# Performance work log

Measured on AMD Instinct MI355X. Metric: run time of the kernel, lower is better.

The kernel has to match this reference:

```python
import jax, jax.numpy as jnp
import numpy as np

GFD = 4096   # global feature dim (VGG fc7)
DH = 1024    # 2 * hidden_dim


def setup_inputs() -> dict:
    key = jax.random.key(0)
    ks = jax.random.split(key, 10)
    b, t_k = 32, 196
    s = lambda fan_in: 1.0 / np.sqrt(fan_in)
    return {
        "global_features": jax.random.normal(ks[0], (b, t_k, GFD), jnp.float32),
        "s_t_hat": jax.random.normal(ks[1], (b, DH), jnp.float32),
        "coverage_img": jnp.zeros((b, t_k, 1), jnp.float32),
        # params
        "Wg": jax.random.normal(ks[2], (GFD, GFD), jnp.float32) * s(GFD),
        "bg": jnp.zeros((GFD,), jnp.float32),
        "Gs": jax.random.normal(ks[3], (GFD, DH), jnp.float32) * s(GFD),
        "bgs": jnp.zeros((DH,), jnp.float32),
        "Wgs": jax.random.normal(ks[4], (DH, DH), jnp.float32) * s(DH),  # w_g_star, no bias
        "Wdec": jax.random.normal(ks[5], (DH, DH), jnp.float32) * s(DH),  # decode_proj
        "bdec": jnp.zeros((DH,), jnp.float32),
        "v": jax.random.normal(ks[6], (DH, 1), jnp.float32) * s(DH),  # score vector, no bias
    }


def reference(global_features, s_t_hat, coverage_img, Wg, bg, Gs, bgs, Wgs, Wdec, bdec, v):
    # g_star: project 4096-d region features -> 1024-d   [b, t_k, DH]
    g1 = global_features @ Wg + bg
    g_star = g1 @ Gs + bgs
    # additive (Bahdanau) scores with coverage
    w_g_star = g_star @ Wgs                       # [b, t_k, DH]
    dec_fea = s_t_hat @ Wdec + bdec               # [b, DH]
    e_a = jnp.tanh(w_g_star + dec_fea[:, None, :] + coverage_img)  # [b, t_k, DH]
    scores = e_a @ v                              # [b, t_k, 1]
    alpha_a = jax.nn.softmax(scores, axis=1)      # softmax over regions
    # attention-weighted context (the bmm)
    c_img = jnp.einsum("bt,btd->bd", alpha_a[..., 0], g_star)  # [b, DH]
    coverage_new = coverage_img + alpha_a
    return c_img, coverage_new, alpha_a
```

## Files before the change

kernel.cpp:

```cpp
#include <hip/hip_runtime.h>
#include <hip/hip_bf16.h>

typedef __attribute__((ext_vector_type(8))) short short8;
typedef __attribute__((ext_vector_type(4))) float floatx4;

#define GLOBAL_AS __attribute__((address_space(1)))
#define LDS_AS    __attribute__((address_space(3)))

__device__ __forceinline__ unsigned short f2bf_rne(float x) {
  unsigned int u = __float_as_uint(x);
  u += 0x7fffu + ((u >> 16) & 1u);
  return (unsigned short)(u >> 16);
}

__global__ void cast_f32_bf16_kernel(const float* __restrict__ in,
                                     unsigned short* __restrict__ out, int n8) {
  int i = blockIdx.x * 256 + threadIdx.x;
  if (i >= n8) return;
  const float4* p = (const float4*)in;
  float4 v0 = p[2 * i], v1 = p[2 * i + 1];
  short8 o;
  o[0] = (short)f2bf_rne(v0.x); o[1] = (short)f2bf_rne(v0.y);
  o[2] = (short)f2bf_rne(v0.z); o[3] = (short)f2bf_rne(v0.w);
  o[4] = (short)f2bf_rne(v1.x); o[5] = (short)f2bf_rne(v1.y);
  o[6] = (short)f2bf_rne(v1.z); o[7] = (short)f2bf_rne(v1.w);
  *(short8*)(out + 8 * (size_t)i) = o;
}

__global__ void transpose_cast_kernel(const float* __restrict__ in,
                                      unsigned short* __restrict__ out, int R, int C) {
  __shared__ unsigned short tile[32][33];
  int tx = threadIdx.x & 31, ty = threadIdx.x >> 5;
  int r0 = blockIdx.y * 32, c0 = blockIdx.x * 32;
#pragma unroll
  for (int j = 0; j < 32; j += 8)
    tile[ty + j][tx] = f2bf_rne(in[(size_t)(r0 + ty + j) * C + c0 + tx]);
  __syncthreads();
#pragma unroll
  for (int j = 0; j < 32; j += 8)
    out[(size_t)(c0 + ty + j) * R + r0 + tx] = tile[tx][ty + j];
}

__global__ void zero4_kernel(float* __restrict__ p, int n4) {
  int i = blockIdx.x * 256 + threadIdx.x;
  if (i < n4) ((float4*)p)[i] = make_float4(0.f, 0.f, 0.f, 0.f);
}
__global__ void init_vec_kernel(const float* __restrict__ src, float* __restrict__ dst) {
  int i = blockIdx.x * 256 + threadIdx.x;
  dst[i] = src[i];
}
__global__ void bias1_accum_kernel(const float* __restrict__ bg, const float* __restrict__ Gs,
                                   float* __restrict__ bias1) {
  int j = blockIdx.x * 256 + threadIdx.x;
  int k0 = blockIdx.y * 256;
  float acc = 0.f;
  for (int k = 0; k < 256; ++k) acc += bg[k0 + k] * Gs[(size_t)(k0 + k) * 1024 + j];
  atomicAdd(&bias1[j], acc);
}

__global__ void init_dec_kernel(const float* __restrict__ bdec, float* __restrict__ dec) {
  int i = blockIdx.x * 256 + threadIdx.x;
  dec[i] = bdec[i & 1023];
}
__global__ void dec_accum_kernel(const float* __restrict__ sth, const float* __restrict__ Wdec,
                                 float* __restrict__ dec) {
  __shared__ float ss[32][128];
  const int tid = threadIdx.x;
  const int k0 = blockIdx.y * 128;
  for (int i = tid; i < 32 * 128; i += 256) {
    int bb = i >> 7, kk = i & 127;
    ss[bb][kk] = sth[bb * 1024 + k0 + kk];
  }
  __syncthreads();
  const int j = blockIdx.x * 256 + tid;
  float acc[32];
#pragma unroll
  for (int b = 0; b < 32; ++b) acc[b] = 0.f;
  for (int kk = 0; kk < 128; ++kk) {
    float w = Wdec[(size_t)(k0 + kk) * 1024 + j];
#pragma unroll
    for (int b = 0; b < 32; ++b) acc[b] += ss[b][kk] * w;
  }
  for (int b = 0; b < 32; ++b) atomicAdd(&dec[b * 1024 + j], acc[b]);
}

template <int BM, int BN, bool HAS_BIAS, bool WRITE_F32, bool WRITE_BF16, bool SWAPXY>
__global__ __launch_bounds__(256, 2) void gemm_tile_kernel(
    const unsigned short* __restrict__ A, const unsigned short* __restrict__ BT,
    const float* __restrict__ bias, float* __restrict__ Cf,
    unsigned short* __restrict__ Cb, int M, int N, int K) {
  constexpr int AF = BM / 32;
  constexpr int BF = BN / 32;
  constexpr int ASLAB = BM * 64;
  constexpr int BSLAB = BN * 64;
  constexpr int ABUF = 2 * ASLAB;
  constexpr int BBUF = 2 * BSLAB;
  __shared__ unsigned short lds_a[BM * 128];
  __shared__ unsigned short lds_b[BN * 128];
  const int tid = threadIdx.x;
  const int lane = tid & 63;
  const int wave = tid >> 6;
  const int wm = wave >> 1, wn = wave & 1;
  const int quad = lane >> 4, col = lane & 15;

  const int gx = (int)gridDim.x;
  const int nwg = gx * (int)gridDim.y;
  const int bid = (int)blockIdx.y * gx + (int)blockIdx.x;
  const int swz = (bid & 7) * (nwg >> 3) + (bid >> 3);
  const int bx = swz % gx, by = swz / gx;
  const int m0 = (SWAPXY ? bx : by) * BM;
  const int n0 = (SWAPXY ? by : bx) * BN;

  floatx4 acc[AF][BF] = {};

  const int srow = tid >> 2;
  const int skoff = (tid & 3) * 8;
  const unsigned short* a_ptr = A + (size_t)(m0 + srow) * K + skoff;
  const unsigned short* b_ptr = BT + (size_t)(n0 + srow) * K + skoff;
  const size_t rowskip = (size_t)64 * K;
  char* const la_dst = (char*)lds_a + tid * 16;
  char* const lb_dst = (char*)lds_b + tid * 16;

#pragma unroll
  for (int h = 0; h < BM / 64; ++h)
#pragma unroll
    for (int s = 0; s < 2; ++s)
      __builtin_amdgcn_global_load_lds((const GLOBAL_AS void*)(a_ptr + h * rowskip + s * 32),
                                       (LDS_AS void*)(la_dst + s * ASLAB + h * 4096), 16, 0, 0);
#pragma unroll
  for (int h = 0; h < BN / 64; ++h)
#pragma unroll
    for (int s = 0; s < 2; ++s)
      __builtin_amdgcn_global_load_lds((const GLOBAL_AS void*)(b_ptr + h * rowskip + s * 32),
                                       (LDS_AS void*)(lb_dst + s * BSLAB + h * 4096), 16, 0, 0);
  a_ptr += 64; b_ptr += 64;
  __syncthreads();

  const int NT = K >> 6;
  int cur = 0;
  for (int t = 0; t < NT; ++t) {
    if (t + 1 < NT) {
      char* la = la_dst + (cur ^ 1) * ABUF;
      char* lb = lb_dst + (cur ^ 1) * BBUF;
#pragma unroll
      for (int h = 0; h < BM / 64; ++h)
#pragma unroll
        for (int s = 0; s < 2; ++s)
          __builtin_amdgcn_global_load_lds((const GLOBAL_AS void*)(a_ptr + h * rowskip + s * 32),
                                           (LDS_AS void*)(la + s * ASLAB + h * 4096), 16, 0, 0);
#pragma unroll
      for (int h = 0; h < BN / 64; ++h)
#pragma unroll
        for (int s = 0; s < 2; ++s)
          __builtin_amdgcn_global_load_lds((const GLOBAL_AS void*)(b_ptr + h * rowskip + s * 32),
                                           (LDS_AS void*)(lb + s * BSLAB + h * 4096), 16, 0, 0);
      a_ptr += 64; b_ptr += 64;
    }
    const char* pa = (const char*)lds_a + cur * ABUF;
    const char* pb = (const char*)lds_b + cur * BBUF;
#pragma unroll
    for (int s = 0; s < 2; ++s) {
      short8 af[AF], bf[BF];
#pragma unroll
      for (int tf = 0; tf < AF; ++tf)
        af[tf] = *(const short8*)(pa + s * ASLAB + (wm * (BM / 2) + tf * 16 + col) * 64 + quad * 16);
#pragma unroll
      for (int tf = 0; tf < BF; ++tf)
        bf[tf] = *(const short8*)(pb + s * BSLAB + (wn * (BN / 2) + tf * 16 + col) * 64 + quad * 16);
#pragma unroll
      for (int tm = 0; tm < AF; ++tm)
#pragma unroll
        for (int tn = 0; tn < BF; ++tn)
          acc[tm][tn] = __builtin_amdgcn_mfma_f32_16x16x32_bf16(af[tm], bf[tn], acc[tm][tn], 0, 0, 0);
    }
    __syncthreads();
    cur ^= 1;
  }

#pragma unroll
  for (int tm = 0; tm < AF; ++tm) {
    const int mg = m0 + wm * (BM / 2) + tm * 16 + quad * 4;
#pragma unroll
    for (int tn = 0; tn < BF; ++tn) {
      const int ng = n0 + wn * (BN / 2) + tn * 16 + col;
      const float bv = HAS_BIAS ? bias[ng] : 0.0f;
#pragma unroll
      for (int r = 0; r < 4; ++r) {
        const float val = acc[tm][tn][r] + bv;
        if (WRITE_F32) Cf[(size_t)(mg + r) * N + ng] = val;
        if (WRITE_BF16) Cb[(size_t)(mg + r) * N + ng] = f2bf_rne(val);
      }
    }
  }
}

__global__ __launch_bounds__(256, 2) void gemm_scores_kernel(
    const unsigned short* __restrict__ A, const unsigned short* __restrict__ BT,
    const float* __restrict__ dec, const float* __restrict__ cov,
    const float* __restrict__ v, float* __restrict__ scores, int M, int N, int K) {
  constexpr int ASLAB = 8192, ABUF = 16384;
  constexpr int BSLAB = 4096, BBUF = 8192;
  __shared__ unsigned short lds_a[128 * 128];
  __shared__ unsigned short lds_b[64 * 128];
  const int tid = threadIdx.x;
  const int lane = tid & 63;
  const int wave = tid >> 6;
  const int wm = wave >> 1, wn = wave & 1;
  const int quad = lane >> 4, col = lane & 15;

  const int gx = (int)gridDim.x;
  const int nwg = gx * (int)gridDim.y;
  const int bid = (int)blockIdx.y * gx + (int)blockIdx.x;
  const int swz = (bid & 7) * (nwg >> 3) + (bid >> 3);
  const int m0 = (swz / gx) * 128, n0 = (swz % gx) * 64;

  floatx4 acc[4][2] = {};

  const int srow = tid >> 2;
  const int skoff = (tid & 3) * 8;
  const unsigned short* a_ptr = A + (size_t)(m0 + srow) * K + skoff;
  const unsigned short* b_ptr = BT + (size_t)(n0 + srow) * K + skoff;
  const size_t rowskip = (size_t)64 * K;
  char* const la_dst = (char*)lds_a + tid * 16;
  char* const lb_dst = (char*)lds_b + tid * 16;

#pragma unroll
  for (int h = 0; h < 2; ++h)
#pragma unroll
    for (int s = 0; s < 2; ++s)
      __builtin_amdgcn_global_load_lds((const GLOBAL_AS void*)(a_ptr + h * rowskip + s * 32),
                                       (LDS_AS void*)(la_dst + s * ASLAB + h * 4096), 16, 0, 0);
#pragma unroll
  for (int s = 0; s < 2; ++s)
    __builtin_amdgcn_global_load_lds((const GLOBAL_AS void*)(b_ptr + s * 32),
                                     (LDS_AS void*)(lb_dst + s * BSLAB), 16, 0, 0);
  a_ptr += 64; b_ptr += 64;
  __syncthreads();

  const int NT = K >> 6;
  int cur = 0;
  for (int t = 0; t < NT; ++t) {
    if (t + 1 < NT) {
      char* la = la_dst + (cur ^ 1) * ABUF;
      char* lb = lb_dst + (cur ^ 1) * BBUF;
#pragma unroll
      for (int h = 0; h < 2; ++h)
#pragma unroll
        for (int s = 0; s < 2; ++s)
          __builtin_amdgcn_global_load_lds((const GLOBAL_AS void*)(a_ptr + h * rowskip + s * 32),
                                           (LDS_AS void*)(la + s * ASLAB + h * 4096), 16, 0, 0);
#pragma unroll
      for (int s = 0; s < 2; ++s)
        __builtin_amdgcn_global_load_lds((const GLOBAL_AS void*)(b_ptr + s * 32),
                                         (LDS_AS void*)(lb + s * BSLAB), 16, 0, 0);
      a_ptr += 64; b_ptr += 64;
    }
    const char* pa = (const char*)lds_a + cur * ABUF;
    const char* pb = (const char*)lds_b + cur * BBUF;
#pragma unroll
    for (int s = 0; s < 2; ++s) {
      short8 af[4], bf[2];
#pragma unroll
      for (int tf = 0; tf < 4; ++tf)
        af[tf] = *(const short8*)(pa + s * ASLAB + (wm * 64 + tf * 16 + col) * 64 + quad * 16);
#pragma unroll
      for (int tf = 0; tf < 2; ++tf)
        bf[tf] = *(const short8*)(pb + s * BSLAB + (wn * 32 + tf * 16 + col) * 64 + quad * 16);
#pragma unroll
      for (int tm = 0; tm < 4; ++tm)
#pragma unroll
        for (int tn = 0; tn < 2; ++tn)
          acc[tm][tn] = __builtin_amdgcn_mfma_f32_16x16x32_bf16(af[tm], bf[tn], acc[tm][tn], 0, 0, 0);
    }
    __syncthreads();
    cur ^= 1;
  }

  const int n_base = n0 + wn * 32;
  float vv[2];
#pragma unroll
  for (int tn = 0; tn < 2; ++tn) vv[tn] = v[n_base + tn * 16 + col];
#pragma unroll
  for (int tm = 0; tm < 4; ++tm) {
#pragma unroll
    for (int r = 0; r < 4; ++r) {
      const int row = m0 + wm * 64 + tm * 16 + quad * 4 + r;
      const int b = row / 196;
      const float cw = cov[row];
      const float* dr = dec + b * 1024 + n_base;
      float s = 0.f;
#pragma unroll
      for (int tn = 0; tn < 2; ++tn)
        s += tanhf(acc[tm][tn][r] + dr[tn * 16 + col] + cw) * vv[tn];
      s += __shfl_xor(s, 1, 64);
      s += __shfl_xor(s, 2, 64);
      s += __shfl_xor(s, 4, 64);
      s += __shfl_xor(s, 8, 64);
      if ((lane & 15) == 0) atomicAdd(&scores[row], s);
    }
  }
}

__global__ void softmax_kernel(const float* __restrict__ scores, const float* __restrict__ cov,
                               float* __restrict__ alpha_ws, float* __restrict__ out) {
  const int b = blockIdx.x, tid = threadIdx.x;
  const int lane = tid & 63, wid = tid >> 6;
  __shared__ float red[8];
  float s = (tid < 196) ? scores[b * 196 + tid] : -1e30f;
  float m = s;
  for (int off = 32; off > 0; off >>= 1) m = fmaxf(m, __shfl_xor(m, off, 64));
  if (lane == 0) red[wid] = m;
  __syncthreads();
  m = fmaxf(fmaxf(red[0], red[1]), fmaxf(red[2], red[3]));
  float e = (tid < 196) ? __expf(s - m) : 0.f;
  float t = e;
  for (int off = 32; off > 0; off >>= 1) t += __shfl_xor(t, off, 64);
  if (lane == 0) red[4 + wid] = t;
  __syncthreads();
  const float tot = red[4] + red[5] + red[6] + red[7];
  const float a = e / tot;
  if (tid < 196) {
    alpha_ws[b * 196 + tid] = a;
    out[32768 + b * 196 + tid] = cov[b * 196 + tid] + a;
    out[32768 + 6272 + b * 196 + tid] = a;
  }
}

__global__ __launch_bounds__(256) void ctx_kernel(const float* __restrict__ alpha,
                                                  const float* __restrict__ gstar,
                                                  float* __restrict__ out) {
  const int b = blockIdx.y;
  const int colbase = blockIdx.x * 128;
  const int c = threadIdx.x & 127;
  const int half = threadIdx.x >> 7;
  const float* g = gstar + ((size_t)b * 196 + half * 98) * 1024 + colbase + c;
  const float* al = alpha + b * 196 + half * 98;
  float acc = 0.f;
#pragma unroll 7
  for (int t = 0; t < 98; ++t) acc += al[t] * g[(size_t)t * 1024];
  __shared__ float part[256];
  part[threadIdx.x] = acc;
  __syncthreads();
  if (threadIdx.x < 128)
    out[b * 1024 + colbase + threadIdx.x] = part[threadIdx.x] + part[threadIdx.x + 128];
}

extern "C" void kernel_launch(void* const* d_in, const int* in_sizes, int n_in,
                              void* d_out, int out_size, void* d_ws, size_t ws_size,
                              hipStream_t stream) {
  (void)in_sizes; (void)n_in; (void)out_size; (void)ws_size;
  const float* gf   = (const float*)d_in[0];
  const float* sth  = (const float*)d_in[1];
  const float* cov  = (const float*)d_in[2];
  const float* Wg   = (const float*)d_in[3];
  const float* bg   = (const float*)d_in[4];
  const float* Gs   = (const float*)d_in[5];
  const float* bgs  = (const float*)d_in[6];
  const float* Wgs  = (const float*)d_in[7];
  const float* Wdec = (const float*)d_in[8];
  const float* bdec = (const float*)d_in[9];
  const float* v    = (const float*)d_in[10];
  float* out = (float*)d_out;

  char* ws = (char*)d_ws;
  unsigned short* gf_bf   = (unsigned short*)(ws + 0);
  float*          alpha   = (float*)(ws + 0);
  unsigned short* Wg_bf   = (unsigned short*)(ws + 51380224);
  float*          gstar_f = (float*)(ws + 51380224);
  unsigned short* GsT     = (unsigned short*)(ws + 84934656);
  unsigned short* WgsT    = (unsigned short*)(ws + 84934656);
  unsigned short* C1T_b   = (unsigned short*)(ws + 93323264);
  unsigned short* gstar_b = (unsigned short*)(ws + 101711872);
  float*          bias1   = (float*)(ws + 114556928);
  float*          dec     = (float*)(ws + 114561024);
  float*          scores  = (float*)(ws + 114692096);

  cast_f32_bf16_kernel<<<12544, 256, 0, stream>>>(gf, gf_bf, 3211264);
  cast_f32_bf16_kernel<<<8192, 256, 0, stream>>>(Wg, Wg_bf, 2097152);
  transpose_cast_kernel<<<dim3(32, 128), 256, 0, stream>>>(Gs, GsT, 4096, 1024);
  init_vec_kernel<<<4, 256, 0, stream>>>(bgs, bias1);
  bias1_accum_kernel<<<dim3(4, 16), 256, 0, stream>>>(bg, Gs, bias1);
  gemm_tile_kernel<128, 64, false, false, true, true><<<dim3(8, 64), 256, 0, stream>>>(
      GsT, Wg_bf, nullptr, nullptr, C1T_b, 1024, 4096, 4096);
  transpose_cast_kernel<<<dim3(32, 32), 256, 0, stream>>>(Wgs, WgsT, 1024, 1024);
  init_dec_kernel<<<128, 256, 0, stream>>>(bdec, dec);
  dec_accum_kernel<<<dim3(4, 8), 256, 0, stream>>>(sth, Wdec, dec);
  gemm_tile_kernel<128, 128, true, true, true, false><<<dim3(8, 49), 256, 0, stream>>>(
      gf_bf, C1T_b, bias1, gstar_f, gstar_b, 6272, 1024, 4096);
  zero4_kernel<<<2, 256, 0, stream>>>(scores, 392);
  gemm_scores_kernel<<<dim3(16, 49), 256, 0, stream>>>(
      gstar_b, WgsT, dec, cov, v, scores, 6272, 1024, 1024);
  softmax_kernel<<<32, 256, 0, stream>>>(scores, cov, alpha, out);
  ctx_kernel<<<dim3(8, 32), 256, 0, stream>>>(alpha, gstar_f, out);
}
```

Before: 505.7 us.

## Deepen GEMM prefetch pipeline to triple-buffer one operand with explicit vmcnt waits

Replaces the double-buffered LDS staging in the GEMM kernels with an asymmetric pipeline that keeps one operand triple-buffered, so it is prefetched two K-steps ahead. Each iteration waits only on the loads it needs, using explicit s_waitcnt vmcnt immediates plus raw s_barrier, instead of a full __syncthreads. This is meant to hide more global-load latency behind the MFMA work. In exchange it uses more LDS per block, which can lower occupancy, and it relies on hand-computed vmcnt encodings.

New measurement: 515.0 us. No clear change (+1.8%).

```diff
diff --git a/kernel.cpp b/kernel.cpp
--- a/kernel.cpp
+++ b/kernel.cpp
@@ -84,19 +84,29 @@
   for (int b = 0; b < 32; ++b) atomicAdd(&dec[b * 1024 + j], acc[b]);
 }
 
-template <int BM, int BN, bool HAS_BIAS, bool WRITE_F32, bool WRITE_BF16, bool SWAPXY>
-__global__ __launch_bounds__(256, 2) void gemm_tile_kernel(
+#define VMCNT_IMM(n) (0x0F70 | ((n) & 15) | ((((n) >> 4) & 3) << 14))
+
+template <int BM, int BN, bool DEEP_A, bool HAS_BIAS, bool WRITE_F32, bool WRITE_BF16,
+          bool SWAPXY>
+__global__ __launch_bounds__(256, 2) void gemm_pipe_kernel(
     const unsigned short* __restrict__ A, const unsigned short* __restrict__ BT,
     const float* __restrict__ bias, float* __restrict__ Cf,
     unsigned short* __restrict__ Cb, int M, int N, int K) {
   constexpr int AF = BM / 32;
   constexpr int BF = BN / 32;
+  constexpr int LA = (BM / 64) * 2;
+  constexpr int LB = (BN / 64) * 2;
   constexpr int ASLAB = BM * 64;
   constexpr int BSLAB = BN * 64;
   constexpr int ABUF = 2 * ASLAB;
   constexpr int BBUF = 2 * BSLAB;
-  __shared__ unsigned short lds_a[BM * 128];
-  __shared__ unsigned short lds_b[BN * 128];
+  constexpr int NBA = DEEP_A ? 3 : 2;
+  constexpr int NBB = DEEP_A ? 2 : 3;
+  constexpr int W_STEADY = VMCNT_IMM(DEEP_A ? (2 * LA + LB) : (LA + 2 * LB));
+  constexpr int W_PEEL = VMCNT_IMM(LA + LB);
+  constexpr int W_ZERO = VMCNT_IMM(0);
+  __shared__ unsigned short lds_a[BM * 64 * NBA];
+  __shared__ unsigned short lds_b[BN * 64 * NBB];
   const int tid = threadIdx.x;
   const int lane = tid & 63;
   const int wave = tid >> 6;
@@ -121,43 +131,50 @@
   char* const la_dst = (char*)lds_a + tid * 16;
   char* const lb_dst = (char*)lds_b + tid * 16;
 
-#pragma unroll
-  for (int h = 0; h < BM / 64; ++h)
-#pragma unroll
-    for (int s = 0; s < 2; ++s)
-      __builtin_amdgcn_global_load_lds((const GLOBAL_AS void*)(a_ptr + h * rowskip + s * 32),
-                                       (LDS_AS void*)(la_dst + s * ASLAB + h * 4096), 16, 0, 0);
-#pragma unroll
-  for (int h = 0; h < BN / 64; ++h)
-#pragma unroll
-    for (int s = 0; s < 2; ++s)
-      __builtin_amdgcn_global_load_lds((const GLOBAL_AS void*)(b_ptr + h * rowskip + s * 32),
-                                       (LDS_AS void*)(lb_dst + s * BSLAB + h * 4096), 16, 0, 0);
-  a_ptr += 64; b_ptr += 64;
-  __syncthreads();
+  auto STAGE_A = [&](int bufoff) {
+#pragma unroll
+    for (int h = 0; h < BM / 64; ++h)
+#pragma unroll
+      for (int s = 0; s < 2; ++s)
+        __builtin_amdgcn_global_load_lds(
+            (const GLOBAL_AS void*)(a_ptr + h * rowskip + s * 32),
+            (LDS_AS void*)(la_dst + bufoff + s * ASLAB + h * 4096), 16, 0, 0);
+    a_ptr += 64;
+  };
+  auto STAGE_B = [&](int bufoff) {
+#pragma unroll
+    for (int h = 0; h < BN / 64; ++h)
+#pragma unroll
+      for (int s = 0; s < 2; ++s)
+        __builtin_amdgcn_global_load_lds(
+            (const GLOBAL_AS void*)(b_ptr + h * rowskip + s * 32),
+            (LDS_AS void*)(lb_dst + bufoff + s * BSLAB + h * 4096), 16, 0, 0);
+    b_ptr += 64;
+  };
+
+  if (DEEP_A) { STAGE_B(0); STAGE_A(0); STAGE_A(ABUF); }
+  else        { STAGE_A(0); STAGE_B(0); STAGE_B(BBUF); }
+  int sa = DEEP_A ? 2 * ABUF : ABUF;
+  int sb = DEEP_A ? BBUF : 2 * BBUF;
+  int ra = 0, rb = 0;
 
   const int NT = K >> 6;
-  int cur = 0;
   for (int t = 0; t < NT; ++t) {
-    if (t + 1 < NT) {
-      char* la = la_dst + (cur ^ 1) * ABUF;
-      char* lb = lb_dst + (cur ^ 1) * BBUF;
-#pragma unroll
-      for (int h = 0; h < BM / 64; ++h)
-#pragma unroll
-        for (int s = 0; s < 2; ++s)
-          __builtin_amdgcn_global_load_lds((const GLOBAL_AS void*)(a_ptr + h * rowskip + s * 32),
-                                           (LDS_AS void*)(la + s * ASLAB + h * 4096), 16, 0, 0);
-#pragma unroll
-      for (int h = 0; h < BN / 64; ++h)
-#pragma unroll
-        for (int s = 0; s < 2; ++s)
-          __builtin_amdgcn_global_load_lds((const GLOBAL_AS void*)(b_ptr + h * rowskip + s * 32),
-                                           (LDS_AS void*)(lb + s * BSLAB + h * 4096), 16, 0, 0);
-      a_ptr += 64; b_ptr += 64;
+    if (DEEP_A) {
+      if (t + 1 < NT) { STAGE_B(sb); sb = (sb == (NBB - 1) * BBUF) ? 0 : sb + BBUF; }
+      if (t + 2 < NT) { STAGE_A(sa); sa = (sa == (NBA - 1) * ABUF) ? 0 : sa + ABUF; }
+    } else {
+      if (t + 1 < NT) { STAGE_A(sa); sa = (sa == (NBA - 1) * ABUF) ? 0 : sa + ABUF; }
+      if (t + 2 < NT) { STAGE_B(sb); sb = (sb == (NBB - 1) * BBUF) ? 0 : sb + BBUF; }
     }
-    const char* pa = (const char*)lds_a + cur * ABUF;
-    const char* pb = (const char*)lds_b + cur * BBUF;
+    if (t < NT - 2)       __builtin_amdgcn_s_waitcnt(W_STEADY);
+    else if (t == NT - 2) __builtin_amdgcn_s_waitcnt(W_PEEL);
+    else                  __builtin_amdgcn_s_waitcnt(W_ZERO);
+    __builtin_amdgcn_s_barrier();
+    asm volatile("" ::: "memory");
+    __builtin_amdgcn_sched_barrier(0);
+    const char* pa = (const char*)lds_a + ra;
+    const char* pb = (const char*)lds_b + rb;
 #pragma unroll
     for (int s = 0; s < 2; ++s) {
       short8 af[AF], bf[BF];
@@ -173,8 +190,11 @@
         for (int tn = 0; tn < BF; ++tn)
           acc[tm][tn] = __builtin_amdgcn_mfma_f32_16x16x32_bf16(af[tm], bf[tn], acc[tm][tn], 0, 0, 0);
     }
-    __syncthreads();
-    cur ^= 1;
+    __builtin_amdgcn_sched_barrier(0);
+    asm volatile("" ::: "memory");
+    __builtin_amdgcn_s_barrier();
+    ra = (ra == (NBA - 1) * ABUF) ? 0 : ra + ABUF;
+    rb = (rb == (NBB - 1) * BBUF) ? 0 : rb + BBUF;
   }
 
 #pragma unroll
@@ -198,10 +218,14 @@
     const unsigned short* __restrict__ A, const unsigned short* __restrict__ BT,
     const float* __restrict__ dec, const float* __restrict__ cov,
     const float* __restrict__ v, float* __restrict__ scores, int M, int N, int K) {
+  constexpr int LA = 4, LB = 2;
   constexpr int ASLAB = 8192, ABUF = 16384;
   constexpr int BSLAB = 4096, BBUF = 8192;
-  __shared__ unsigned short lds_a[128 * 128];
-  __shared__ unsigned short lds_b[64 * 128];
+  constexpr int W_STEADY = VMCNT_IMM(2 * LA + LB);
+  constexpr int W_PEEL = VMCNT_IMM(LA + LB);
+  constexpr int W_ZERO = VMCNT_IMM(0);
+  __shared__ unsigned short lds_a[128 * 64 * 3];
+  __shared__ unsigned short lds_b[64 * 64 * 2];
   const int tid = threadIdx.x;
   const int lane = tid & 63;
   const int wave = tid >> 6;
@@ -224,39 +248,41 @@
   char* const la_dst = (char*)lds_a + tid * 16;
   char* const lb_dst = (char*)lds_b + tid * 16;
 
-#pragma unroll
-  for (int h = 0; h < 2; ++h)
+  auto STAGE_A = [&](int bufoff) {
+#pragma unroll
+    for (int h = 0; h < 2; ++h)
+#pragma unroll
+      for (int s = 0; s < 2; ++s)
+        __builtin_amdgcn_global_load_lds(
+            (const GLOBAL_AS void*)(a_ptr + h * rowskip + s * 32),
+            (LDS_AS void*)(la_dst + bufoff + s * ASLAB + h * 4096), 16, 0, 0);
+    a_ptr += 64;
+  };
+  auto STAGE_B = [&](int bufoff) {
 #pragma unroll
     for (int s = 0; s < 2; ++s)
-      __builtin_amdgcn_global_load_lds((const GLOBAL_AS void*)(a_ptr + h * rowskip + s * 32),
-                                       (LDS_AS void*)(la_dst + s * ASLAB + h * 4096), 16, 0, 0);
-#pragma unroll
-  for (int s = 0; s < 2; ++s)
-    __builtin_amdgcn_global_load_lds((const GLOBAL_AS void*)(b_ptr + s * 32),
-                                     (LDS_AS void*)(lb_dst + s * BSLAB), 16, 0, 0);
-  a_ptr += 64; b_ptr += 64;
-  __syncthreads();
+      __builtin_amdgcn_global_load_lds(
+          (const GLOBAL_AS void*)(b_ptr + s * 32),
+          (LDS_AS void*)(lb_dst + bufoff + s * BSLAB), 16, 0, 0);
+    b_ptr += 64;
+  };
+
+  STAGE_B(0); STAGE_A(0); STAGE_A(ABUF);
+  int sa = 2 * ABUF, sb = BBUF;
+  int ra = 0, rb = 0;
 
   const int NT = K >> 6;
-  int cur = 0;
   for (int t = 0; t < NT; ++t) {
-    if (t + 1 < NT) {
-      char* la = la_dst + (cur ^ 1) * ABUF;
-      char* lb = lb_dst + (cur ^ 1) * BBUF;
-#pragma unroll
-      for (int h = 0; h < 2; ++h)
-#pragma unroll
-        for (int s = 0; s < 2; ++s)
-          __builtin_amdgcn_global_load_lds((const GLOBAL_AS void*)(a_ptr + h * rowskip + s * 32),
-                                           (LDS_AS void*)(la + s * ASLAB + h * 4096), 16, 0, 0);
-#pragma unroll
-      for (int s = 0; s < 2; ++s)
-        __builtin_amdgcn_global_load_lds((const GLOBAL_AS void*)(b_ptr + s * 32),
-                                         (LDS_AS void*)(lb + s * BSLAB), 16, 0, 0);
-      a_ptr += 64; b_ptr += 64;
-    }
-    const char* pa = (const char*)lds_a + cur * ABUF;
-    const char* pb = (const char*)lds_b + cur * BBUF;
+    if (t + 1 < NT) { STAGE_B(sb); sb = (sb == BBUF) ? 0 : BBUF; }
+    if (t + 2 < NT) { STAGE_A(sa); sa = (sa == 2 * ABUF) ? 0 : sa + ABUF; }
+    if (t < NT - 2)       __builtin_amdgcn_s_waitcnt(W_STEADY);
+    else if (t == NT - 2) __builtin_amdgcn_s_waitcnt(W_PEEL);
+    else                  __builtin_amdgcn_s_waitcnt(W_ZERO);
+    __builtin_amdgcn_s_barrier();
+    asm volatile("" ::: "memory");
+    __builtin_amdgcn_sched_barrier(0);
+    const char* pa = (const char*)lds_a + ra;
+    const char* pb = (const char*)lds_b + rb;
 #pragma unroll
     for (int s = 0; s < 2; ++s) {
       short8 af[4], bf[2];
@@ -272,8 +298,11 @@
         for (int tn = 0; tn < 2; ++tn)
           acc[tm][tn] = __builtin_amdgcn_mfma_f32_16x16x32_bf16(af[tm], bf[tn], acc[tm][tn], 0, 0, 0);
     }
-    __syncthreads();
-    cur ^= 1;
+    __builtin_amdgcn_sched_barrier(0);
+    asm volatile("" ::: "memory");
+    __builtin_amdgcn_s_barrier();
+    ra = (ra == 2 * ABUF) ? 0 : ra + ABUF;
+    rb = (rb == BBUF) ? 0 : BBUF;
   }
 
   const int n_base = n0 + wn * 32;
@@ -380,12 +409,12 @@
   transpose_cast_kernel<<<dim3(32, 128), 256, 0, stream>>>(Gs, GsT, 4096, 1024);
   init_vec_kernel<<<4, 256, 0, stream>>>(bgs, bias1);
   bias1_accum_kernel<<<dim3(4, 16), 256, 0, stream>>>(bg, Gs, bias1);
-  gemm_tile_kernel<128, 64, false, false, true, true><<<dim3(8, 64), 256, 0, stream>>>(
+  gemm_pipe_kernel<128, 64, false, false, false, true, true><<<dim3(8, 64), 256, 0, stream>>>(
       GsT, Wg_bf, nullptr, nullptr, C1T_b, 1024, 4096, 4096);
   transpose_cast_kernel<<<dim3(32, 32), 256, 0, stream>>>(Wgs, WgsT, 1024, 1024);
   init_dec_kernel<<<128, 256, 0, stream>>>(bdec, dec);
   dec_accum_kernel<<<dim3(4, 8), 256, 0, stream>>>(sth, Wdec, dec);
-  gemm_tile_kernel<128, 128, true, true, true, false><<<dim3(8, 49), 256, 0, stream>>>(
+  gemm_pipe_kernel<128, 128, true, true, true, true, false><<<dim3(8, 49), 256, 0, stream>>>(
       gf_bf, C1T_b, bias1, gstar_f, gstar_b, 6272, 1024, 4096);
   zero4_kernel<<<2, 256, 0, stream>>>(scores, 392);
   gemm_scores_kernel<<<dim3(16, 49), 256, 0, stream>>>(
```

## Split-K the g_star GEMM, merge prep kernels, and rewrite decoder projection

Applied to the files above, without the earlier changes.

Small prep launches are merged into two multi-role kernels (casts, transposes, bias folding, decoder projection, score zeroing). The decoder projection is rewritten to skip atomics, and the bias init becomes a device memcpy. The main 6272x1024x4096 GEMM now splits K across two z-slices to raise workgroup count from 392 to 784. A reduce kernel then sums the partials, adds bias and writes the fp32 and bf16 copies of g_star. This adds extra fp32 partial write/read traffic in exchange for better occupancy and fewer launches.

New measurement: 683.6 us. 1.35x slower.

```diff
diff --git a/kernel.cpp b/kernel.cpp
--- a/kernel.cpp
+++ b/kernel.cpp
@@ -2,6 +2,7 @@
 #include <hip/hip_bf16.h>
 
 typedef __attribute__((ext_vector_type(8))) short short8;
+typedef __attribute__((ext_vector_type(4))) short short4v;
 typedef __attribute__((ext_vector_type(4))) float floatx4;
 
 #define GLOBAL_AS __attribute__((address_space(1)))
@@ -13,9 +14,10 @@
   return (unsigned short)(u >> 16);
 }
 
-__global__ void cast_f32_bf16_kernel(const float* __restrict__ in,
-                                     unsigned short* __restrict__ out, int n8) {
-  int i = blockIdx.x * 256 + threadIdx.x;
+__device__ __forceinline__ void cast8_body(const float* __restrict__ in,
+                                           unsigned short* __restrict__ out,
+                                           int blk, int n8) {
+  int i = blk * 256 + threadIdx.x;
   if (i >= n8) return;
   const float4* p = (const float4*)in;
   float4 v0 = p[2 * i], v1 = p[2 * i + 1];
@@ -27,11 +29,12 @@
   *(short8*)(out + 8 * (size_t)i) = o;
 }
 
-__global__ void transpose_cast_kernel(const float* __restrict__ in,
-                                      unsigned short* __restrict__ out, int R, int C) {
+__device__ __forceinline__ void trans32_body(const float* __restrict__ in,
+                                             unsigned short* __restrict__ out,
+                                             int R, int C, int bx, int by) {
   __shared__ unsigned short tile[32][33];
   int tx = threadIdx.x & 31, ty = threadIdx.x >> 5;
-  int r0 = blockIdx.y * 32, c0 = blockIdx.x * 32;
+  int r0 = by * 32, c0 = bx * 32;
 #pragma unroll
   for (int j = 0; j < 32; j += 8)
     tile[ty + j][tx] = f2bf_rne(in[(size_t)(r0 + ty + j) * C + c0 + tx]);
@@ -41,54 +44,80 @@
     out[(size_t)(c0 + ty + j) * R + r0 + tx] = tile[tx][ty + j];
 }
 
-__global__ void zero4_kernel(float* __restrict__ p, int n4) {
-  int i = blockIdx.x * 256 + threadIdx.x;
-  if (i < n4) ((float4*)p)[i] = make_float4(0.f, 0.f, 0.f, 0.f);
-}
-__global__ void init_vec_kernel(const float* __restrict__ src, float* __restrict__ dst) {
-  int i = blockIdx.x * 256 + threadIdx.x;
-  dst[i] = src[i];
-}
-__global__ void bias1_accum_kernel(const float* __restrict__ bg, const float* __restrict__ Gs,
-                                   float* __restrict__ bias1) {
-  int j = blockIdx.x * 256 + threadIdx.x;
-  int k0 = blockIdx.y * 256;
-  float acc = 0.f;
-  for (int k = 0; k < 256; ++k) acc += bg[k0 + k] * Gs[(size_t)(k0 + k) * 1024 + j];
-  atomicAdd(&bias1[j], acc);
-}
-
-__global__ void init_dec_kernel(const float* __restrict__ bdec, float* __restrict__ dec) {
-  int i = blockIdx.x * 256 + threadIdx.x;
-  dec[i] = bdec[i & 1023];
-}
-__global__ void dec_accum_kernel(const float* __restrict__ sth, const float* __restrict__ Wdec,
-                                 float* __restrict__ dec) {
-  __shared__ float ss[32][128];
-  const int tid = threadIdx.x;
-  const int k0 = blockIdx.y * 128;
-  for (int i = tid; i < 32 * 128; i += 256) {
-    int bb = i >> 7, kk = i & 127;
-    ss[bb][kk] = sth[bb * 1024 + k0 + kk];
-  }
-  __syncthreads();
-  const int j = blockIdx.x * 256 + tid;
-  float acc[32];
-#pragma unroll
-  for (int b = 0; b < 32; ++b) acc[b] = 0.f;
-  for (int kk = 0; kk < 128; ++kk) {
-    float w = Wdec[(size_t)(k0 + kk) * 1024 + j];
-#pragma unroll
-    for (int b = 0; b < 32; ++b) acc[b] += ss[b][kk] * w;
-  }
-  for (int b = 0; b < 32; ++b) atomicAdd(&dec[b * 1024 + j], acc[b]);
-}
-
-template <int BM, int BN, bool HAS_BIAS, bool WRITE_F32, bool WRITE_BF16, bool SWAPXY>
+__global__ void prep1_kernel(const float* __restrict__ gf, unsigned short* __restrict__ gf_bf,
+                             const float* __restrict__ Wg, unsigned short* __restrict__ Wg_bf,
+                             const float* __restrict__ Gs, unsigned short* __restrict__ GsT,
+                             const float* __restrict__ bg, float* __restrict__ bias1) {
+  const int b = blockIdx.x;
+  if (b < 12544) {
+    cast8_body(gf, gf_bf, b, 3211264);
+  } else if (b < 20736) {
+    cast8_body(Wg, Wg_bf, b - 12544, 2097152);
+  } else if (b < 24832) {
+    int bb = b - 20736;
+    trans32_body(Gs, GsT, 4096, 1024, bb & 31, bb >> 5);
+  } else {
+    int bb = b - 24832;
+    int j = (bb & 3) * 256 + threadIdx.x;
+    int k0 = (bb >> 2) * 256;
+    float acc = 0.f;
+    for (int k = 0; k < 256; ++k) acc += bg[k0 + k] * Gs[(size_t)(k0 + k) * 1024 + j];
+    atomicAdd(&bias1[j], acc);
+  }
+}
+
+__global__ void prep2_kernel(const float* __restrict__ Wgs, unsigned short* __restrict__ WgsT,
+                             const float* __restrict__ sth, const float* __restrict__ Wdec,
+                             const float* __restrict__ bdec, float* __restrict__ dec,
+                             float* __restrict__ scores) {
+  const int b = blockIdx.x;
+  if (b < 1024) {
+    trans32_body(Wgs, WgsT, 1024, 1024, b & 31, b >> 5);
+  } else if (b < 1040) {
+    int bb = b - 1024;
+    int j = (bb & 3) * 256 + threadIdx.x;
+    int r0 = (bb >> 2) * 8;
+    float acc[8];
+    const float bd = bdec[j];
+#pragma unroll
+    for (int r = 0; r < 8; ++r) acc[r] = bd;
+    for (int k = 0; k < 1024; ++k) {
+      float w = Wdec[(size_t)k * 1024 + j];
+#pragma unroll
+      for (int r = 0; r < 8; ++r) acc[r] += sth[(r0 + r) * 1024 + k] * w;
+    }
+#pragma unroll
+    for (int r = 0; r < 8; ++r) dec[(r0 + r) * 1024 + j] = acc[r];
+  } else {
+    int i = (b - 1040) * 256 + threadIdx.x;
+    if (i < 1568) ((float4*)scores)[i] = make_float4(0.f, 0.f, 0.f, 0.f);
+  }
+}
+
+__global__ __launch_bounds__(256) void reduce2_kernel(const float* __restrict__ p0,
+                                                      const float* __restrict__ p1,
+                                                      const float* __restrict__ bias,
+                                                      float* __restrict__ gf32,
+                                                      unsigned short* __restrict__ gb16) {
+  const int i = blockIdx.x * 256 + threadIdx.x;
+  float4 a = ((const float4*)p0)[i];
+  float4 b = ((const float4*)p1)[i];
+  float4 bv = ((const float4*)bias)[i & 255];
+  float4 r;
+  r.x = a.x + b.x + bv.x; r.y = a.y + b.y + bv.y;
+  r.z = a.z + b.z + bv.z; r.w = a.w + b.w + bv.w;
+  ((float4*)gf32)[i] = r;
+  short4v o;
+  o[0] = (short)f2bf_rne(r.x); o[1] = (short)f2bf_rne(r.y);
+  o[2] = (short)f2bf_rne(r.z); o[3] = (short)f2bf_rne(r.w);
+  *(short4v*)(gb16 + 4 * (size_t)i) = o;
+}
+
+template <int BM, int BN, bool WRITE_F32, bool WRITE_BF16, bool SWAPXY>
 __global__ __launch_bounds__(256, 2) void gemm_tile_kernel(
     const unsigned short* __restrict__ A, const unsigned short* __restrict__ BT,
-    const float* __restrict__ bias, float* __restrict__ Cf,
-    unsigned short* __restrict__ Cb, int M, int N, int K) {
+    float* __restrict__ Cf, unsigned short* __restrict__ Cb,
+    int M, int N, int K, int Ksub, size_t csplit) {
   constexpr int AF = BM / 32;
   constexpr int BF = BN / 32;
   constexpr int ASLAB = BM * 64;
@@ -110,13 +139,14 @@
   const int bx = swz % gx, by = swz / gx;
   const int m0 = (SWAPXY ? bx : by) * BM;
   const int n0 = (SWAPXY ? by : bx) * BN;
+  const int kb = (int)blockIdx.z * Ksub;
 
   floatx4 acc[AF][BF] = {};
 
   const int srow = tid >> 2;
   const int skoff = (tid & 3) * 8;
-  const unsigned short* a_ptr = A + (size_t)(m0 + srow) * K + skoff;
-  const unsigned short* b_ptr = BT + (size_t)(n0 + srow) * K + skoff;
+  const unsigned short* a_ptr = A + (size_t)(m0 + srow) * K + kb + skoff;
+  const unsigned short* b_ptr = BT + (size_t)(n0 + srow) * K + kb + skoff;
   const size_t rowskip = (size_t)64 * K;
   char* const la_dst = (char*)lds_a + tid * 16;
   char* const lb_dst = (char*)lds_b + tid * 16;
@@ -136,7 +166,7 @@
   a_ptr += 64; b_ptr += 64;
   __syncthreads();
 
-  const int NT = K >> 6;
+  const int NT = Ksub >> 6;
   int cur = 0;
   for (int t = 0; t < NT; ++t) {
     if (t + 1 < NT) {
@@ -177,17 +207,17 @@
     cur ^= 1;
   }
 
+  float* Cfz = Cf + (size_t)blockIdx.z * csplit;
 #pragma unroll
   for (int tm = 0; tm < AF; ++tm) {
     const int mg = m0 + wm * (BM / 2) + tm * 16 + quad * 4;
 #pragma unroll
     for (int tn = 0; tn < BF; ++tn) {
       const int ng = n0 + wn * (BN / 2) + tn * 16 + col;
-      const float bv = HAS_BIAS ? bias[ng] : 0.0f;
 #pragma unroll
       for (int r = 0; r < 4; ++r) {
-        const float val = acc[tm][tn][r] + bv;
-        if (WRITE_F32) Cf[(size_t)(mg + r) * N + ng] = val;
+        const float val = acc[tm][tn][r];
+        if (WRITE_F32) Cfz[(size_t)(mg + r) * N + ng] = val;
         if (WRITE_BF16) Cb[(size_t)(mg + r) * N + ng] = f2bf_rne(val);
       }
     }
@@ -364,30 +394,27 @@
 
   char* ws = (char*)d_ws;
   unsigned short* gf_bf   = (unsigned short*)(ws + 0);
-  float*          alpha   = (float*)(ws + 0);
+  unsigned short* gstar_b = (unsigned short*)(ws + 0);
   unsigned short* Wg_bf   = (unsigned short*)(ws + 51380224);
+  float*          p0      = (float*)(ws + 51380224);
   float*          gstar_f = (float*)(ws + 51380224);
+  float*          p1      = (float*)(ws + 77070336);
   unsigned short* GsT     = (unsigned short*)(ws + 84934656);
-  unsigned short* WgsT    = (unsigned short*)(ws + 84934656);
-  unsigned short* C1T_b   = (unsigned short*)(ws + 93323264);
-  unsigned short* gstar_b = (unsigned short*)(ws + 101711872);
-  float*          bias1   = (float*)(ws + 114556928);
-  float*          dec     = (float*)(ws + 114561024);
-  float*          scores  = (float*)(ws + 114692096);
-
-  cast_f32_bf16_kernel<<<12544, 256, 0, stream>>>(gf, gf_bf, 3211264);
-  cast_f32_bf16_kernel<<<8192, 256, 0, stream>>>(Wg, Wg_bf, 2097152);
-  transpose_cast_kernel<<<dim3(32, 128), 256, 0, stream>>>(Gs, GsT, 4096, 1024);
-  init_vec_kernel<<<4, 256, 0, stream>>>(bgs, bias1);
-  bias1_accum_kernel<<<dim3(4, 16), 256, 0, stream>>>(bg, Gs, bias1);
-  gemm_tile_kernel<128, 64, false, false, true, true><<<dim3(8, 64), 256, 0, stream>>>(
-      GsT, Wg_bf, nullptr, nullptr, C1T_b, 1024, 4096, 4096);
-  transpose_cast_kernel<<<dim3(32, 32), 256, 0, stream>>>(Wgs, WgsT, 1024, 1024);
-  init_dec_kernel<<<128, 256, 0, stream>>>(bdec, dec);
-  dec_accum_kernel<<<dim3(4, 8), 256, 0, stream>>>(sth, Wdec, dec);
-  gemm_tile_kernel<128, 128, true, true, true, false><<<dim3(8, 49), 256, 0, stream>>>(
-      gf_bf, C1T_b, bias1, gstar_f, gstar_b, 6272, 1024, 4096);
-  zero4_kernel<<<2, 256, 0, stream>>>(scores, 392);
+  unsigned short* C1T_b   = (unsigned short*)(ws + 102760448);
+  unsigned short* WgsT    = (unsigned short*)(ws + 111149056);
+  float*          bias1   = (float*)(ws + 113246208);
+  float*          dec     = (float*)(ws + 113262592);
+  float*          scores  = (float*)(ws + 113393664);
+  float*          alpha   = (float*)(ws + 113426432);
+
+  hipMemcpyAsync(bias1, bgs, 4096, hipMemcpyDeviceToDevice, stream);
+  prep1_kernel<<<24896, 256, 0, stream>>>(gf, gf_bf, Wg, Wg_bf, Gs, GsT, bg, bias1);
+  gemm_tile_kernel<128, 64, false, true, true><<<dim3(8, 64, 1), 256, 0, stream>>>(
+      GsT, Wg_bf, nullptr, C1T_b, 1024, 4096, 4096, 4096, 0);
+  prep2_kernel<<<1047, 256, 0, stream>>>(Wgs, WgsT, sth, Wdec, bdec, dec, scores);
+  gemm_tile_kernel<128, 128, true, false, false><<<dim3(8, 49, 2), 256, 0, stream>>>(
+      gf_bf, C1T_b, p0, nullptr, 6272, 1024, 4096, 2048, 6422528);
+  reduce2_kernel<<<6272, 256, 0, stream>>>(p0, p1, bias1, gstar_f, gstar_b);
   gemm_scores_kernel<<<dim3(16, 49), 256, 0, stream>>>(
       gstar_b, WgsT, dec, cov, v, scores, 6272, 1024, 1024);
   softmax_kernel<<<32, 256, 0, stream>>>(scores, cov, alpha, out);
```
